# Performance work log

Hardware: AMD Instinct MI355X
Metric: run time of the kernel (lower is better)

Reference implementation:

```python
import jax, jax.numpy as jnp
import numpy as np

N = 100000      # nodes
E = 1600000     # edges (avg degree 16)
D_IN = 128
D_OUT = 128
ORDER = 2
EPS = 1e-9


def setup_inputs() -> dict:
    key = jax.random.key(0)
    ks = jax.random.split(key, 8)
    inp = {}
    inp["vecs"] = jax.random.normal(ks[0], (N, D_IN), dtype=jnp.float32)
    inp["adj_vals"] = jax.random.uniform(ks[1], (E,), dtype=jnp.float32)
    inp["row"] = jax.random.randint(ks[2], (E,), 0, N)
    inp["col"] = jax.random.randint(ks[3], (E,), 0, N)
    lim = float(np.sqrt(6.0 / (D_IN + D_OUT)))  # glorot uniform
    for o in range(ORDER + 1):
        inp[f"W{o}"] = jax.random.uniform(ks[4 + o], (D_IN, D_OUT), dtype=jnp.float32, minval=-lim, maxval=lim)
        inp[f"b{o}"] = jnp.zeros((D_OUT,), jnp.float32)
        inp[f"off{o}"] = jnp.zeros((1, D_OUT), jnp.float32)
        inp[f"sc{o}"] = jnp.ones((1, D_OUT), jnp.float32)
    return inp


def _spmm(vals, row, col, x):
    # sparse_tensor_dense_matmul: out[r] = sum_e vals[e] * x[col[e]] for row[e]==r
    return jax.ops.segment_sum(vals[:, None] * x[col], row, num_segments=N)


def _f_nonlinear(v, W, b, off, sc):
    vw = jax.nn.relu(v @ W + b)
    mean = jnp.mean(vw, axis=1, keepdims=True)
    var = jnp.var(vw, axis=1, keepdims=True)
    # tf.nn.batch_normalization with per-row moments, eps=1e-9
    return sc * (vw - mean) * jax.lax.rsqrt(var + EPS) + off


def reference(vecs, adj_vals, row, col,
              W0, W1, W2, b0, b1, b2,
              off0, off1, off2, sc0, sc1, sc2):
    Ws = [W0, W1, W2]
    bs = [b0, b1, b2]
    offs = [off0, off1, off2]
    scs = [sc0, sc1, sc2]
    # vecs_hop[k] = A^k @ vecs (dropout=0 -> identity)
    hops = [vecs]
    for _ in range(ORDER):
        hops.append(_spmm(adj_vals, row, col, hops[-1]))
    outs = [_f_nonlinear(hops[o], Ws[o], bs[o], offs[o], scs[o]) for o in range(ORDER + 1)]
    ret = outs[0]
    for o in range(1, ORDER + 1):  # aggr == 'mean' (actually a sum in the source)
        ret = ret + outs[o]
    return ret
```

## Files before the change

kernel.cpp:

```cpp
#include <hip/hip_runtime.h>
#include <math.h>

#define NN 100000
#define DD 128
#define NB 391
#define RP_PAD 100004

typedef short bf16x8 __attribute__((ext_vector_type(8)));
typedef float f32x4  __attribute__((ext_vector_type(4)));
typedef unsigned uint4v __attribute__((ext_vector_type(4)));

__device__ __forceinline__ unsigned f2bf_rne(float f) {
    unsigned u = __float_as_uint(f);
    return (u + 0x7FFFu + ((u >> 16) & 1u)) >> 16;
}
__device__ __forceinline__ unsigned packbf(float a, float b) {
    return f2bf_rne(a) | (f2bf_rne(b) << 16);
}
__device__ __forceinline__ float bf_lo(unsigned u) { return __uint_as_float(u << 16); }
__device__ __forceinline__ float bf_hi(unsigned u) { return __uint_as_float(u & 0xFFFF0000u); }

__device__ __forceinline__ int2 ldnt_edge(const int2* p) {
    long long v = __builtin_nontemporal_load((const long long*)p);
    int2 r;
    r.x = (int)(v & 0xffffffffll);
    r.y = (int)(((unsigned long long)v) >> 32);
    return r;
}

__global__ __launch_bounds__(1024) void scatter_convert(
    const int* __restrict__ row, const int* __restrict__ col,
    const float* __restrict__ vals, int* __restrict__ bcnt,
    int2* __restrict__ ep_raw, int E, int CAP, int cb,
    const float* __restrict__ vecs, unsigned short* __restrict__ vecs_bf,
    const float* __restrict__ W0, const float* __restrict__ W1,
    const float* __restrict__ W2, unsigned short* __restrict__ Wt, int n8)
{
    const int b = blockIdx.x;
    const int t = threadIdx.x;

    if (b >= cb) {
        const int b2 = b - cb;
        if (b2 < 6) {
            const int m = b2 >> 1;
            const float* W = (m == 0) ? W0 : ((m == 1) ? W1 : W2);
            unsigned short* dst = Wt + m * DD * DD;
            int idx = (b2 & 1) * 1024 + t;
            int n = idx >> 4;
            int kc = (idx & 15) * 8;
            unsigned r[4];
            #pragma unroll
            for (int j = 0; j < 4; j++) {
                float a = W[(kc + 2 * j) * DD + n];
                float c = W[(kc + 2 * j + 1) * DD + n];
                r[j] = packbf(a, c);
            }
            *(uint4*)(dst + n * DD + kc) = make_uint4(r[0], r[1], r[2], r[3]);
        } else {
            int i = (b2 - 6) * 1024 + t;
            if (i >= n8) return;
            f32x4 a = __builtin_nontemporal_load((const f32x4*)vecs + (size_t)i * 2);
            f32x4 c = __builtin_nontemporal_load((const f32x4*)vecs + (size_t)i * 2 + 1);
            uint4v o;
            o.x = packbf(a.x, a.y); o.y = packbf(a.z, a.w);
            o.z = packbf(c.x, c.y); o.w = packbf(c.z, c.w);
            ((uint4v*)vecs_bf)[i] = o;
        }
        return;
    }

    __shared__ int cnt[NB];
    __shared__ int base[NB];
    if (t < NB) cnt[t] = 0;
    __syncthreads();
    const int eb = b * 8192;
    const int ee = min(eb + 8192, E);

    int   rr[8];
    int   cc[8];
    float vv[8];
    #pragma unroll
    for (int i = 0; i < 8; i++) {
        int j = eb + t + i * 1024;
        rr[i] = -1;
        if (j < ee) {
            rr[i] = row[j];
            cc[i] = __builtin_nontemporal_load(col + j);
            vv[i] = __builtin_nontemporal_load(vals + j);
            atomicAdd(&cnt[rr[i] >> 8], 1);
        }
    }
    __syncthreads();
    if (t < NB) {
        int c = cnt[t];
        base[t] = c ? (t * CAP + atomicAdd(&bcnt[t], c)) : 0;
        cnt[t] = 0;
    }
    __syncthreads();
    #pragma unroll
    for (int i = 0; i < 8; i++) {
        int r = rr[i];
        if (r >= 0) {
            int bk = r >> 8;
            int off = atomicAdd(&cnt[bk], 1);
            unsigned meta = (unsigned)cc[i] | ((unsigned)(r & 255) << 17);
            ep_raw[base[bk] + off] = make_int2((int)meta, __float_as_int(vv[i]));
        }
    }
}

__global__ __launch_bounds__(1024) void csr_compact(
    const int* __restrict__ bcnt, const int2* __restrict__ ep_raw,
    int* __restrict__ row_ptr, int2* __restrict__ ep,
    int CAP, int N, int E)
{
    __shared__ int red[1024];
    __shared__ int rcnt[256];
    __shared__ int rcur[256];
    __shared__ int wsum[4];
    const int b = blockIdx.x;
    const int t = threadIdx.x;

    int part = 0;
    for (int j = t; j < b; j += 1024) part += bcnt[j];
    red[t] = part;
    __syncthreads();
    #pragma unroll
    for (int off = 512; off > 0; off >>= 1) {
        if (t < off) red[t] += red[t + off];
        __syncthreads();
    }
    const int dst = red[0];
    const int cnt = bcnt[b];
    const int src = b * CAP;

    if (t < 256) rcnt[t] = 0;
    __syncthreads();
    for (int j = t; j < cnt; j += 1024)
        atomicAdd(&rcnt[(unsigned)ep_raw[src + j].x >> 17], 1);
    __syncthreads();

    int v = 0, inc = 0;
    const int lane = t & 63;
    if (t < 256) {
        v = rcnt[t];
        inc = v;
        #pragma unroll
        for (int off = 1; off < 64; off <<= 1) {
            int u = __shfl_up(inc, off, 64);
            if (lane >= off) inc += u;
        }
        if (lane == 63) wsum[t >> 6] = inc;
    }
    __syncthreads();
    if (t < 256) {
        int woff = 0;
        for (int i = 0; i < (t >> 6); i++) woff += wsum[i];
        int excl = woff + inc - v;
        int grow = b * 256 + t;
        if (grow < N) row_ptr[grow] = dst + excl;
        rcur[t] = excl;
    }
    __syncthreads();

    for (int j = t; j < cnt; j += 1024) {
        int2 rec = ldnt_edge(ep_raw + src + j);
        unsigned meta = (unsigned)rec.x;
        int rlo = meta >> 17;
        int c = (int)(meta & 0x1FFFFu);
        int p = atomicAdd(&rcur[rlo], 1);
        ep[dst + p] = make_int2(c, rec.y);
    }
    if (b == 0 && t == 0) row_ptr[N] = E;
}

__device__ __forceinline__ void accum8(float* acc, uint4 u, float v) {
    acc[0] += v * bf_lo(u.x); acc[1] += v * bf_hi(u.x);
    acc[2] += v * bf_lo(u.y); acc[3] += v * bf_hi(u.y);
    acc[4] += v * bf_lo(u.z); acc[5] += v * bf_hi(u.z);
    acc[6] += v * bf_lo(u.w); acc[7] += v * bf_hi(u.w);
}

__global__ __launch_bounds__(256) void spmm_bf16(
    const uint4* __restrict__ x, const int* __restrict__ row_ptr,
    const int2* __restrict__ ep, uint4* __restrict__ out, int N)
{
    int t = blockIdx.x * 256 + threadIdx.x;
    int g = t >> 4;
    int lane = t & 15;
    if (g >= N) return;

    int s = row_ptr[g];
    int e = row_ptr[g + 1];
    float acc[8] = {0.f, 0.f, 0.f, 0.f, 0.f, 0.f, 0.f, 0.f};

    int k = s;
    for (; k + 8 <= e; k += 8) {
        int2 E0 = ep[k + 0], E1 = ep[k + 1], E2 = ep[k + 2], E3 = ep[k + 3];
        int2 E4 = ep[k + 4], E5 = ep[k + 5], E6 = ep[k + 6], E7 = ep[k + 7];
        uint4 X0 = x[(size_t)E0.x * 16 + lane];
        uint4 X1 = x[(size_t)E1.x * 16 + lane];
        uint4 X2 = x[(size_t)E2.x * 16 + lane];
        uint4 X3 = x[(size_t)E3.x * 16 + lane];
        uint4 X4 = x[(size_t)E4.x * 16 + lane];
        uint4 X5 = x[(size_t)E5.x * 16 + lane];
        uint4 X6 = x[(size_t)E6.x * 16 + lane];
        uint4 X7 = x[(size_t)E7.x * 16 + lane];
        accum8(acc, X0, __int_as_float(E0.y));
        accum8(acc, X1, __int_as_float(E1.y));
        accum8(acc, X2, __int_as_float(E2.y));
        accum8(acc, X3, __int_as_float(E3.y));
        accum8(acc, X4, __int_as_float(E4.y));
        accum8(acc, X5, __int_as_float(E5.y));
        accum8(acc, X6, __int_as_float(E6.y));
        accum8(acc, X7, __int_as_float(E7.y));
    }
    for (; k + 4 <= e; k += 4) {
        int2 E0 = ep[k + 0], E1 = ep[k + 1], E2 = ep[k + 2], E3 = ep[k + 3];
        uint4 X0 = x[(size_t)E0.x * 16 + lane];
        uint4 X1 = x[(size_t)E1.x * 16 + lane];
        uint4 X2 = x[(size_t)E2.x * 16 + lane];
        uint4 X3 = x[(size_t)E3.x * 16 + lane];
        accum8(acc, X0, __int_as_float(E0.y));
        accum8(acc, X1, __int_as_float(E1.y));
        accum8(acc, X2, __int_as_float(E2.y));
        accum8(acc, X3, __int_as_float(E3.y));
    }
    for (; k < e; k++) {
        int2 E0 = ep[k];
        uint4 X0 = x[(size_t)E0.x * 16 + lane];
        accum8(acc, X0, __int_as_float(E0.y));
    }

    uint4 o;
    o.x = packbf(acc[0], acc[1]); o.y = packbf(acc[2], acc[3]);
    o.z = packbf(acc[4], acc[5]); o.w = packbf(acc[6], acc[7]);
    out[(size_t)g * 16 + lane] = o;
}

__device__ __forceinline__ void bn_accum(
    f32x4* acc, const float* __restrict__ bias, const float* __restrict__ off,
    const float* __restrict__ sc, int i, float facc[8][4])
{
    float bc[8], sv[8], ov[8];
    #pragma unroll
    for (int ct = 0; ct < 8; ct++) {
        int c = ct * 16 + i;
        bc[ct] = bias[c]; sv[ct] = sc[c]; ov[ct] = off[c];
    }
    float s[4] = {0.f, 0.f, 0.f, 0.f};
    float qq[4] = {0.f, 0.f, 0.f, 0.f};
    #pragma unroll
    for (int ct = 0; ct < 8; ct++) {
        #pragma unroll
        for (int r = 0; r < 4; r++) {
            float v = fmaxf(acc[ct][r] + bc[ct], 0.f);
            acc[ct][r] = v;
            s[r] += v;
            qq[r] += v * v;
        }
    }
    #pragma unroll
    for (int r = 0; r < 4; r++) {
        #pragma unroll
        for (int m = 1; m <= 8; m <<= 1) {
            s[r]  += __shfl_xor(s[r],  m, 64);
            qq[r] += __shfl_xor(qq[r], m, 64);
        }
    }
    #pragma unroll
    for (int r = 0; r < 4; r++) {
        float mn = s[r] * 0.0078125f;
        float var = qq[r] * 0.0078125f - mn * mn;
        float rs = rsqrtf(var + 1e-9f);
        #pragma unroll
        for (int ct = 0; ct < 8; ct++)
            facc[ct][r] += sv[ct] * (acc[ct][r] - mn) * rs + ov[ct];
    }
}

__global__ __launch_bounds__(256) void fused_dense_mfma(
    const unsigned short* __restrict__ h0,
    const unsigned short* __restrict__ h1,
    const unsigned short* __restrict__ h2,
    const unsigned short* __restrict__ Wt,
    const float* __restrict__ b0, const float* __restrict__ b1,
    const float* __restrict__ b2,
    const float* __restrict__ off0, const float* __restrict__ off1,
    const float* __restrict__ off2,
    const float* __restrict__ sc0, const float* __restrict__ sc1,
    const float* __restrict__ sc2,
    float* __restrict__ out, int N)
{
    __shared__ uint4 Bl[2048];

    const int tid  = threadIdx.x;
    const int wave = tid >> 6;
    const int lane = tid & 63;
    const int i    = lane & 15;
    const int q    = lane >> 4;
    const int slab = blockIdx.x * 64 + wave * 16;

    int arow = slab + i;
    if (arow >= N) arow = N - 1;

    const unsigned short* hops[3] = {h0, h1, h2};
    const float* bs[3]  = {b0, b1, b2};
    const float* ofs[3] = {off0, off1, off2};
    const float* scs[3] = {sc0, sc1, sc2};
    const bf16x8* Bv = (const bf16x8*)Bl;

    float facc[8][4];
    #pragma unroll
    for (int ct = 0; ct < 8; ct++)
        #pragma unroll
        for (int r = 0; r < 4; r++) facc[ct][r] = 0.f;

    for (int o = 0; o < 3; o++) {
        const uint4* Wg = (const uint4*)(Wt + o * DD * DD);
        #pragma unroll
        for (int j = 0; j < 8; j++) {
            int c  = j * 256 + tid;
            int nn = c & 127;
            int kc = c >> 7;
            Bl[kc * 128 + nn] = Wg[nn * 16 + kc];
        }
        __syncthreads();

        const unsigned short* arow_p = hops[o] + (size_t)arow * DD + q * 8;
        f32x4 acc[8];
        #pragma unroll
        for (int ct = 0; ct < 8; ct++) acc[ct] = (f32x4){0.f, 0.f, 0.f, 0.f};
        #pragma unroll
        for (int kb = 0; kb < 4; kb++) {
            bf16x8 a = __builtin_nontemporal_load((const bf16x8*)(arow_p + kb * 32));
            const int kc = kb * 4 + q;
            #pragma unroll
            for (int ct = 0; ct < 8; ct++) {
                bf16x8 b = Bv[kc * 128 + ct * 16 + i];
                acc[ct] = __builtin_amdgcn_mfma_f32_16x16x32_bf16(a, b, acc[ct], 0, 0, 0);
            }
        }
        bn_accum(acc, bs[o], ofs[o], scs[o], i, facc);
        __syncthreads();
    }

    #pragma unroll
    for (int r = 0; r < 4; r++) {
        int orow = slab + q * 4 + r;
        if (orow < N) {
            float* op = out + (size_t)orow * DD + i;
            #pragma unroll
            for (int ct = 0; ct < 8; ct++)
                __builtin_nontemporal_store(facc[ct][r], op + ct * 16);
        }
    }
}

extern "C" void kernel_launch(void* const* d_in, const int* in_sizes, int n_in,
                              void* d_out, int out_size, void* d_ws, size_t ws_size,
                              hipStream_t stream)
{
    const float* vecs = (const float*)d_in[0];
    const float* adj  = (const float*)d_in[1];
    const int*   row  = (const int*)d_in[2];
    const int*   col  = (const int*)d_in[3];
    const float* W0   = (const float*)d_in[4];
    const float* b0   = (const float*)d_in[5];
    const float* off0 = (const float*)d_in[6];
    const float* sc0  = (const float*)d_in[7];
    const float* W1   = (const float*)d_in[8];
    const float* b1   = (const float*)d_in[9];
    const float* off1 = (const float*)d_in[10];
    const float* sc1  = (const float*)d_in[11];
    const float* W2   = (const float*)d_in[12];
    const float* b2   = (const float*)d_in[13];
    const float* off2 = (const float*)d_in[14];
    const float* sc2  = (const float*)d_in[15];

    const int E = in_sizes[1];
    const int N = NN;

    const int avg = (E + NB - 1) / NB;
    const int CAP = (avg + 8 * (int)sqrt((double)avg) + 79) & ~15;

    unsigned short* hop1_bf = (unsigned short*)d_ws;
    unsigned short* hop2_bf = hop1_bf + (size_t)N * DD;
    unsigned short* vecs_bf = hop2_bf + (size_t)N * DD;
    unsigned short* Wt_bf   = vecs_bf + (size_t)N * DD;
    int*   row_ptr  = (int*)(Wt_bf + 3 * DD * DD);
    int*   bcnt     = row_ptr + RP_PAD;
    int2*  ep_raw   = (int2*)(bcnt + 512);
    int2*  epack    = ep_raw + (size_t)NB * CAP;

    hipMemsetAsync(bcnt, 0, NB * sizeof(int), stream);

    const int cb = (E + 8191) / 8192;
    const int n8 = N * DD / 8;
    const int vb = (n8 + 1023) / 1024;
    scatter_convert<<<cb + 6 + vb, 1024, 0, stream>>>(
        row, col, adj, bcnt, ep_raw, E, CAP, cb,
        vecs, vecs_bf, W0, W1, W2, Wt_bf, n8);

    csr_compact<<<NB, 1024, 0, stream>>>(
        bcnt, ep_raw, row_ptr, epack, CAP, N, E);

    int sb = (N * 16 + 255) / 256;
    spmm_bf16<<<sb, 256, 0, stream>>>(
        (const uint4*)vecs_bf, row_ptr, epack, (uint4*)hop1_bf, N);
    spmm_bf16<<<sb, 256, 0, stream>>>(
        (const uint4*)hop1_bf, row_ptr, epack, (uint4*)hop2_bf, N);

    const int db = (N + 63) / 64;
    fused_dense_mfma<<<db, 256, 0, stream>>>(
        vecs_bf, hop1_bf, hop2_bf, Wt_bf,
        b0, b1, b2, off0, off1, off2, sc0, sc1, sc2,
        (float*)d_out, N);
}
```

Measured before the change: 337.2 us.

## Overlap per-order dense MFMA work with SpMM gather kernels via interleaved blocks

Splits the fused three-order dense kernel into per-order pieces. Dense order 0 and order 1 each run inside an SpMM launch, with every fifth block doing dense work. The aim is to hide dense compute behind the memory-bound gather. The trade-off is that the fp32 output is now read and written repeatedly, a read-modify-write per order, which adds substantial global traffic.

```diff
diff --git a/kernel.cpp b/kernel.cpp
--- a/kernel.cpp
+++ b/kernel.cpp
@@ -181,19 +181,11 @@
     acc[6] += v * bf_lo(u.w); acc[7] += v * bf_hi(u.w);
 }
 
-__global__ __launch_bounds__(256) void spmm_bf16(
-    const uint4* __restrict__ x, const int* __restrict__ row_ptr,
-    const int2* __restrict__ ep, uint4* __restrict__ out, int N)
-{
-    int t = blockIdx.x * 256 + threadIdx.x;
-    int g = t >> 4;
-    int lane = t & 15;
-    if (g >= N) return;
-
-    int s = row_ptr[g];
-    int e = row_ptr[g + 1];
+__device__ __forceinline__ uint4 row_gather(
+    const uint4* __restrict__ x, const int2* __restrict__ ep,
+    int s, int e, int lane)
+{
     float acc[8] = {0.f, 0.f, 0.f, 0.f, 0.f, 0.f, 0.f, 0.f};
-
     int k = s;
     for (; k + 8 <= e; k += 8) {
         int2 E0 = ep[k + 0], E1 = ep[k + 1], E2 = ep[k + 2], E3 = ep[k + 3];
@@ -231,11 +223,10 @@
         uint4 X0 = x[(size_t)E0.x * 16 + lane];
         accum8(acc, X0, __int_as_float(E0.y));
     }
-
     uint4 o;
     o.x = packbf(acc[0], acc[1]); o.y = packbf(acc[2], acc[3]);
     o.z = packbf(acc[4], acc[5]); o.w = packbf(acc[6], acc[7]);
-    out[(size_t)g * 16 + lane] = o;
+    return o;
 }
 
 __device__ __forceinline__ void bn_accum(
@@ -279,72 +270,72 @@
     }
 }
 
-__global__ __launch_bounds__(256) void fused_dense_mfma(
+__device__ __forceinline__ void dense_order(
+    const unsigned short* __restrict__ h, const uint4* __restrict__ Wg,
+    uint4* Bl, const float* __restrict__ bias,
+    const float* __restrict__ off, const float* __restrict__ sc,
+    int tid, int i, int q, int arow, float facc[8][4])
+{
+    #pragma unroll
+    for (int j = 0; j < 8; j++) {
+        int c  = j * 256 + tid;
+        int nn = c & 127;
+        int kc = c >> 7;
+        Bl[kc * 128 + nn] = Wg[nn * 16 + kc];
+    }
+    __syncthreads();
+    const bf16x8* Bv = (const bf16x8*)Bl;
+    const unsigned short* arow_p = h + (size_t)arow * DD + q * 8;
+    f32x4 acc[8];
+    #pragma unroll
+    for (int ct = 0; ct < 8; ct++) acc[ct] = (f32x4){0.f, 0.f, 0.f, 0.f};
+    #pragma unroll
+    for (int kb = 0; kb < 4; kb++) {
+        bf16x8 a = __builtin_nontemporal_load((const bf16x8*)(arow_p + kb * 32));
+        const int kc = kb * 4 + q;
+        #pragma unroll
+        for (int ct = 0; ct < 8; ct++) {
+            bf16x8 b = Bv[kc * 128 + ct * 16 + i];
+            acc[ct] = __builtin_amdgcn_mfma_f32_16x16x32_bf16(a, b, acc[ct], 0, 0, 0);
+        }
+    }
+    bn_accum(acc, bias, off, sc, i, facc);
+}
+
+__global__ __launch_bounds__(256) void spmm1_dense0(
+    const uint4* __restrict__ xv, const int* __restrict__ row_ptr,
+    const int2* __restrict__ ep, uint4* __restrict__ hop1,
     const unsigned short* __restrict__ h0,
-    const unsigned short* __restrict__ h1,
-    const unsigned short* __restrict__ h2,
     const unsigned short* __restrict__ Wt,
-    const float* __restrict__ b0, const float* __restrict__ b1,
-    const float* __restrict__ b2,
-    const float* __restrict__ off0, const float* __restrict__ off1,
-    const float* __restrict__ off2,
-    const float* __restrict__ sc0, const float* __restrict__ sc1,
-    const float* __restrict__ sc2,
-    float* __restrict__ out, int N)
+    const float* __restrict__ b0, const float* __restrict__ off0,
+    const float* __restrict__ sc0, float* __restrict__ out, int N)
 {
     __shared__ uint4 Bl[2048];
-
-    const int tid  = threadIdx.x;
+    const int q5 = blockIdx.x / 5;
+    const int r5 = blockIdx.x % 5;
+    if (r5 < 4) {
+        int t = (q5 * 4 + r5) * 256 + threadIdx.x;
+        int g = t >> 4;
+        int lane = t & 15;
+        if (g >= N) return;
+        hop1[(size_t)g * 16 + lane] =
+            row_gather(xv, ep, row_ptr[g], row_ptr[g + 1], lane);
+        return;
+    }
+    const int tid = threadIdx.x;
     const int wave = tid >> 6;
     const int lane = tid & 63;
-    const int i    = lane & 15;
-    const int q    = lane >> 4;
-    const int slab = blockIdx.x * 64 + wave * 16;
-
+    const int i = lane & 15;
+    const int q = lane >> 4;
+    const int slab = q5 * 64 + wave * 16;
     int arow = slab + i;
     if (arow >= N) arow = N - 1;
-
-    const unsigned short* hops[3] = {h0, h1, h2};
-    const float* bs[3]  = {b0, b1, b2};
-    const float* ofs[3] = {off0, off1, off2};
-    const float* scs[3] = {sc0, sc1, sc2};
-    const bf16x8* Bv = (const bf16x8*)Bl;
-
     float facc[8][4];
     #pragma unroll
     for (int ct = 0; ct < 8; ct++)
         #pragma unroll
         for (int r = 0; r < 4; r++) facc[ct][r] = 0.f;
-
-    for (int o = 0; o < 3; o++) {
-        const uint4* Wg = (const uint4*)(Wt + o * DD * DD);
-        #pragma unroll
-        for (int j = 0; j < 8; j++) {
-            int c  = j * 256 + tid;
-            int nn = c & 127;
-            int kc = c >> 7;
-            Bl[kc * 128 + nn] = Wg[nn * 16 + kc];
-        }
-        __syncthreads();
-
-        const unsigned short* arow_p = hops[o] + (size_t)arow * DD + q * 8;
-        f32x4 acc[8];
-        #pragma unroll
-        for (int ct = 0; ct < 8; ct++) acc[ct] = (f32x4){0.f, 0.f, 0.f, 0.f};
-        #pragma unroll
-        for (int kb = 0; kb < 4; kb++) {
-            bf16x8 a = __builtin_nontemporal_load((const bf16x8*)(arow_p + kb * 32));
-            const int kc = kb * 4 + q;
-            #pragma unroll
-            for (int ct = 0; ct < 8; ct++) {
-                bf16x8 b = Bv[kc * 128 + ct * 16 + i];
-                acc[ct] = __builtin_amdgcn_mfma_f32_16x16x32_bf16(a, b, acc[ct], 0, 0, 0);
-            }
-        }
-        bn_accum(acc, bs[o], ofs[o], scs[o], i, facc);
-        __syncthreads();
-    }
-
+    dense_order(h0, (const uint4*)Wt, Bl, b0, off0, sc0, tid, i, q, arow, facc);
     #pragma unroll
     for (int r = 0; r < 4; r++) {
         int orow = slab + q * 4 + r;
@@ -353,6 +344,91 @@
             #pragma unroll
             for (int ct = 0; ct < 8; ct++)
                 __builtin_nontemporal_store(facc[ct][r], op + ct * 16);
+        }
+    }
+}
+
+__global__ __launch_bounds__(256) void spmm2_dense1(
+    const uint4* __restrict__ xv, const int* __restrict__ row_ptr,
+    const int2* __restrict__ ep, uint4* __restrict__ hop2,
+    const unsigned short* __restrict__ h1,
+    const unsigned short* __restrict__ Wt,
+    const float* __restrict__ b1, const float* __restrict__ off1,
+    const float* __restrict__ sc1, float* __restrict__ out, int N)
+{
+    __shared__ uint4 Bl[2048];
+    const int q5 = blockIdx.x / 5;
+    const int r5 = blockIdx.x % 5;
+    if (r5 < 4) {
+        int t = (q5 * 4 + r5) * 256 + threadIdx.x;
+        int g = t >> 4;
+        int lane = t & 15;
+        if (g >= N) return;
+        hop2[(size_t)g * 16 + lane] =
+            row_gather(xv, ep, row_ptr[g], row_ptr[g + 1], lane);
+        return;
+    }
+    const int tid = threadIdx.x;
+    const int wave = tid >> 6;
+    const int lane = tid & 63;
+    const int i = lane & 15;
+    const int q = lane >> 4;
+    const int slab = q5 * 64 + wave * 16;
+    int arow = slab + i;
+    if (arow >= N) arow = N - 1;
+    float facc[8][4];
+    #pragma unroll
+    for (int ct = 0; ct < 8; ct++)
+        #pragma unroll
+        for (int r = 0; r < 4; r++) facc[ct][r] = 0.f;
+    dense_order(h1, (const uint4*)(Wt + DD * DD), Bl, b1, off1, sc1,
+                tid, i, q, arow, facc);
+    #pragma unroll
+    for (int r = 0; r < 4; r++) {
+        int orow = slab + q * 4 + r;
+        if (orow < N) {
+            float* op = out + (size_t)orow * DD + i;
+            #pragma unroll
+            for (int ct = 0; ct < 8; ct++) {
+                float prev = op[ct * 16];
+                __builtin_nontemporal_store(prev + facc[ct][r], op + ct * 16);
+            }
+        }
+    }
+}
+
+__global__ __launch_bounds__(256) void dense2_final(
+    const unsigned short* __restrict__ h2,
+    const unsigned short* __restrict__ Wt,
+    const float* __restrict__ b2, const float* __restrict__ off2,
+    const float* __restrict__ sc2, float* __restrict__ out, int N)
+{
+    __shared__ uint4 Bl[2048];
+    const int tid = threadIdx.x;
+    const int wave = tid >> 6;
+    const int lane = tid & 63;
+    const int i = lane & 15;
+    const int q = lane >> 4;
+    const int slab = blockIdx.x * 64 + wave * 16;
+    int arow = slab + i;
+    if (arow >= N) arow = N - 1;
+    float facc[8][4];
+    #pragma unroll
+    for (int ct = 0; ct < 8; ct++)
+        #pragma unroll
+        for (int r = 0; r < 4; r++) facc[ct][r] = 0.f;
+    dense_order(h2, (const uint4*)(Wt + 2 * DD * DD), Bl, b2, off2, sc2,
+                tid, i, q, arow, facc);
+    #pragma unroll
+    for (int r = 0; r < 4; r++) {
+        int orow = slab + q * 4 + r;
+        if (orow < N) {
+            float* op = out + (size_t)orow * DD + i;
+            #pragma unroll
+            for (int ct = 0; ct < 8; ct++) {
+                float prev = op[ct * 16];
+                __builtin_nontemporal_store(prev + facc[ct][r], op + ct * 16);
+            }
         }
     }
 }
@@ -405,15 +481,16 @@
     csr_compact<<<NB, 1024, 0, stream>>>(
         bcnt, ep_raw, row_ptr, epack, CAP, N, E);
 
-    int sb = (N * 16 + 255) / 256;
-    spmm_bf16<<<sb, 256, 0, stream>>>(
-        (const uint4*)vecs_bf, row_ptr, epack, (uint4*)hop1_bf, N);
-    spmm_bf16<<<sb, 256, 0, stream>>>(
-        (const uint4*)hop1_bf, row_ptr, epack, (uint4*)hop2_bf, N);
-
     const int db = (N + 63) / 64;
-    fused_dense_mfma<<<db, 256, 0, stream>>>(
-        vecs_bf, hop1_bf, hop2_bf, Wt_bf,
-        b0, b1, b2, off0, off1, off2, sc0, sc1, sc2,
-        (float*)d_out, N);
-}
+    const int grid = db * 5;
+    spmm1_dense0<<<grid, 256, 0, stream>>>(
+        (const uint4*)vecs_bf, row_ptr, epack, (uint4*)hop1_bf,
+        vecs_bf, Wt_bf, b0, off0, sc0, (float*)d_out, N);
+
+    spmm2_dense1<<<grid, 256, 0, stream>>>(
+        (const uint4*)hop1_bf, row_ptr, epack, (uint4*)hop2_bf,
+        hop1_bf, Wt_bf, b1, off1, sc1, (float*)d_out, N);
+
+    dense2_final<<<db, 256, 0, stream>>>(
+        hop2_bf, Wt_bf, b2, off2, sc2, (float*)d_out, N);
+}
```

Measured after the change: 373.7 us. 10.8% more time.
